# Performance work log

Measured on AMD Instinct MI355X. Metric: run time of the kernel, lower is better.

Reference implementation:

```python
import jax, jax.numpy as jnp
import numpy as np

SHAPE = (4096, 4096)
TAU = 1.0
EPS = 1e-8


def setup_inputs() -> dict:
    key = jax.random.key(0)
    k1, k2, k3 = jax.random.split(key, 3)
    mask_logits = 0.1 * jax.random.normal(k1, SHAPE, dtype=jnp.float32)
    u1 = jax.random.uniform(k2, SHAPE, dtype=jnp.float32)
    u2 = jax.random.uniform(k3, SHAPE + (2,), dtype=jnp.float32)
    return {"mask_logits": mask_logits, "u1": u1, "u2": u2,
            "k": 1677721, "training": 1}


def _gumbel(u):
    # -log(-log(U + eps) + eps), matching the torch code's noise
    return -jnp.log(-jnp.log(u + EPS) + EPS)


def reference(mask_logits, u1, u2, k, training):
    shape = mask_logits.shape
    if training:
        # gumbel-perturbed logits
        logits_with_noise = (mask_logits + _gumbel(u1)) / TAU
        flat = logits_with_noise.reshape(-1)                 # [N]
        _, top_idx = jax.lax.top_k(flat, k)                  # [k]
        # scatter: binary candidate mask (constant values -> non-diff, as in torch)
        mask = jnp.zeros_like(flat).at[top_idx].set(1.0)     # [N]
        # F.gumbel_softmax(stack([0, mask], -1), tau, hard=True)[..., 1]
        logits2 = jnp.stack([jnp.zeros_like(mask), mask], axis=-1)   # [N, 2]
        g2 = _gumbel(u2.reshape(-1, 2))                      # [N, 2]
        y = jax.nn.softmax((logits2 + g2) / TAU, axis=-1)    # soft sample
        hard = jax.nn.one_hot(jnp.argmax(y, axis=-1), 2, dtype=y.dtype)
        out = (hard + y - jax.lax.stop_gradient(y))[..., 1]  # straight-through
        return out.reshape(shape)
    else:
        flat = mask_logits.reshape(-1)
        _, top_idx = jax.lax.top_k(flat, k)
        mask = jnp.zeros_like(flat).at[top_idx].set(1.0)
        return mask.reshape(shape)
```

## Files before the change

kernel.cpp:

```cpp
#include <hip/hip_runtime.h>
#include <hip/hip_bf16.h>
#include <math.h>
#include <cstdint>

#define FEPS 1e-8f
#define NBLK 2048
#define NTHR 256
#define CAND_CAP 4096

#define ZMIN 8.0f
#define ZSCALE 128.0f
#define ZBINW 0.0078125f


__device__ __forceinline__ uint32_t f2k(float f) {
    uint32_t b = __float_as_uint(f);
    return (b & 0x80000000u) ? ~b : (b | 0x80000000u);
}

__device__ __forceinline__ float gum_fast(float u) {
    float t = u + FEPS;
    float a = logf(t);
    float w = -a + FEPS;
    float d = logf(w);
    return -d;
}

__device__ __forceinline__ float logCR(float x) {
    return (float)log((double)x);
}
__device__ __forceinline__ float gum_cr(float u) {
    float t = u + FEPS;
    float a = logCR(t);
    float w = -a + FEPS;
    float d = logCR(w);
    return -d;
}

__device__ __forceinline__ float decide_cr(float maskv, float ua, float ub) {
    float G0 = gum_cr(ua);
    float G1 = gum_cr(ub);
    float V1 = maskv + G1;
    float diff = V1 - G0;
    return (diff > 0x1p-25f) ? 1.0f : 0.0f;
}
__device__ __forceinline__ float decide_tr(float maskv, float ua, float ub) {
    float g0 = gum_fast(ua);
    float g1 = gum_fast(ub);
    float v1 = maskv + g1;
    float diff = v1 - g0;
    if (fabsf(diff) > 1e-4f) return (diff > 0.0f) ? 1.0f : 0.0f;
    return decide_cr(maskv, ua, ub);
}

__device__ __forceinline__ int zbin(float z) {
    float t = (z + ZMIN) * ZSCALE;
    int b = (int)t;
    if (b < 0) b = 0;
    if (b > 4095) b = 4095;
    return b;
}

__global__ void __launch_bounds__(NTHR) k_keys(
        const float* __restrict__ lg, const float* __restrict__ u1,
        const int* __restrict__ trainp, uint32_t* __restrict__ keys,
        uint32_t* __restrict__ hist1, int N) {
    __shared__ uint32_t h[4096];
    for (int b = threadIdx.x; b < 4096; b += blockDim.x) h[b] = 0u;
    __syncthreads();
    const int tr = *trainp;
    const int n4 = N >> 2;
    const int tid = blockIdx.x * blockDim.x + threadIdx.x;
    const int stride = gridDim.x * blockDim.x;
    for (int i = tid; i < n4; i += stride) {
        float4 m = ((const float4*)lg)[i];
        float4 u = ((const float4*)u1)[i];
        float z0, z1, z2, z3;
        if (tr) {
            z0 = m.x + gum_fast(u.x);
            z1 = m.y + gum_fast(u.y);
            z2 = m.z + gum_fast(u.z);
            z3 = m.w + gum_fast(u.w);
        } else { z0 = m.x; z1 = m.y; z2 = m.z; z3 = m.w; }
        uint4 kk = make_uint4(f2k(z0), f2k(z1), f2k(z2), f2k(z3));
        ((uint4*)keys)[i] = kk;
        atomicAdd(&h[zbin(z0)], 1u);
        atomicAdd(&h[zbin(z1)], 1u);
        atomicAdd(&h[zbin(z2)], 1u);
        atomicAdd(&h[zbin(z3)], 1u);
    }
    for (int i = (n4 << 2) + tid; i < N; i += stride) {
        float m = lg[i], u = u1[i];
        float z = tr ? (m + gum_fast(u)) : m;
        keys[i] = f2k(z);
        atomicAdd(&h[zbin(z)], 1u);
    }
    __syncthreads();
    for (int b = threadIdx.x; b < 4096; b += blockDim.x) {
        uint32_t v = h[b];
        if (v) atomicAdd(&hist1[b], v);
    }
}

__global__ void __launch_bounds__(1024) k_scan1(
        const uint32_t* __restrict__ hist1, const int* __restrict__ kptr,
        uint32_t* __restrict__ scal) {
    __shared__ uint32_t vals[4096];
    __shared__ uint32_t cnt[1024];
    const int t = threadIdx.x;
    uint32_t loc = 0;
    for (int j = 0; j < 4; j++) {
        uint32_t v = hist1[4095 - (t * 4 + j)];
        vals[t * 4 + j] = v;
        loc += v;
    }
    cnt[t] = loc;
    __syncthreads();
    for (int off = 1; off < 1024; off <<= 1) {
        uint32_t add = (t >= off) ? cnt[t - off] : 0u;
        __syncthreads();
        cnt[t] += add;
        __syncthreads();
    }
    const uint32_t K = (uint32_t)(*kptr);
    uint32_t excl = (t > 0) ? cnt[t - 1] : 0u;
    uint32_t incl = cnt[t];
    if (excl < K && K <= incl) {
        uint32_t c = excl;
        for (int j = 0; j < 4; j++) {
            uint32_t v = vals[t * 4 + j];
            if (K <= c + v) {
                int b1 = 4095 - (t * 4 + j);
                float edge = (float)b1 * ZBINW - ZMIN;
                uint32_t kb = f2k(edge) - 2048u;
                scal[0] = kb;
                break;
            }
            c += v;
        }
    }
}

__global__ void __launch_bounds__(NTHR) k_hist2(
        const uint32_t* __restrict__ keys, const uint32_t* __restrict__ scal,
        uint32_t* __restrict__ hist2, uint32_t* __restrict__ gtOut, int N) {
    __shared__ uint32_t red[NTHR];
    const uint32_t kb = scal[0];
    const uint32_t hiB = kb + (1u << 20);
    const int n4 = N >> 2;
    const int tid = blockIdx.x * blockDim.x + threadIdx.x;
    const int stride = gridDim.x * blockDim.x;
    uint32_t gt = 0;
    for (int i = tid; i < n4; i += stride) {
        uint4 kk = ((const uint4*)keys)[i];
        uint32_t ks[4] = {kk.x, kk.y, kk.z, kk.w};
        #pragma unroll
        for (int j = 0; j < 4; j++) {
            uint32_t kx = ks[j];
            if (kx >= hiB) gt++;
            else if (kx >= kb) atomicAdd(&hist2[kx - kb], 1u);
        }
    }
    for (int i = (n4 << 2) + tid; i < N; i += stride) {
        uint32_t kx = keys[i];
        if (kx >= hiB) gt++;
        else if (kx >= kb) atomicAdd(&hist2[kx - kb], 1u);
    }
    red[threadIdx.x] = gt;
    __syncthreads();
    for (int off = NTHR / 2; off; off >>= 1) {
        if (threadIdx.x < off) red[threadIdx.x] += red[threadIdx.x + off];
        __syncthreads();
    }
    if (threadIdx.x == 0 && red[0]) atomicAdd(gtOut, red[0]);
}

__global__ void __launch_bounds__(NTHR) k_part(
        const uint32_t* __restrict__ hist2, uint32_t* __restrict__ part) {
    __shared__ uint32_t red[NTHR];
    uint32_t sum = 0;
    const int base = blockIdx.x << 10;
    for (int j = threadIdx.x; j < 1024; j += NTHR) sum += hist2[base + j];
    red[threadIdx.x] = sum;
    __syncthreads();
    for (int off = NTHR / 2; off; off >>= 1) {
        if (threadIdx.x < off) red[threadIdx.x] += red[threadIdx.x + off];
        __syncthreads();
    }
    if (threadIdx.x == 0) part[blockIdx.x] = red[0];
}

__global__ void __launch_bounds__(1024) k_scan2(
        const uint32_t* __restrict__ hist2, const uint32_t* __restrict__ part,
        const int* __restrict__ kptr, uint32_t* __restrict__ scal) {
    __shared__ uint32_t cs[1024];
    __shared__ uint32_t bs[1024];
    __shared__ uint32_t red[1024];
    __shared__ int shI[4];
    const int t = threadIdx.x;
    const uint32_t kb = scal[0];
    const uint32_t GT = scal[1];
    const uint32_t kk1 = (uint32_t)(*kptr) - GT;

    cs[t] = part[1023 - t];
    __syncthreads();
    for (int off = 1; off < 1024; off <<= 1) {
        uint32_t add = (t >= off) ? cs[t - off] : 0u;
        __syncthreads();
        cs[t] += add;
        __syncthreads();
    }
    {
        uint32_t excl = t ? cs[t - 1] : 0u;
        if (excl < kk1 && kk1 <= cs[t]) shI[0] = t;
    }
    __syncthreads();
    const int rp = shI[0];
    const int jc = 1023 - rp;
    const uint32_t gt_chunks = rp ? cs[rp - 1] : 0u;
    const uint32_t kk_in = kk1 - gt_chunks;

    bs[t] = hist2[(jc << 10) + (1023 - t)];
    __syncthreads();
    for (int off = 1; off < 1024; off <<= 1) {
        uint32_t add = (t >= off) ? bs[t - off] : 0u;
        __syncthreads();
        bs[t] += add;
        __syncthreads();
    }
    {
        uint32_t excl = t ? bs[t - 1] : 0u;
        if (excl < kk_in && kk_in <= bs[t]) shI[1] = t;
    }
    __syncthreads();
    const int rq = shI[1];
    const int b2 = (jc << 10) + (1023 - rq);

    int W = 64;
    int lo = 0, hi = 0;
    uint32_t caw = 0;
    while (true) {
        lo = b2 - W; if (lo < 0) lo = 0;
        hi = b2 + W; if (hi > 0xFFFFF) hi = 0xFFFFF;
        uint32_t v = 0;
        for (int b = lo + t; b <= hi; b += 1024) v += hist2[b];
        red[t] = v;
        __syncthreads();
        for (int off = 512; off; off >>= 1) {
            if (t < off) red[t] += red[t + off];
            __syncthreads();
        }
        uint32_t nW = red[0];
        __syncthreads();
        if (nW <= 3500u || W == 0) {
            const int ch = hi >> 10;
            const int chend = (ch << 10) + 1023;
            uint32_t v2 = 0;
            for (int b = hi + 1 + t; b <= chend; b += 1024) v2 += hist2[b];
            red[t] = v2;
            __syncthreads();
            for (int off = 512; off; off >>= 1) {
                if (t < off) red[t] += red[t + off];
                __syncthreads();
            }
            uint32_t inpart = red[0];
            __syncthreads();
            const int rpch = 1023 - ch;
            const uint32_t sufExcl = rpch ? cs[rpch - 1] : 0u;
            caw = GT + sufExcl + inpart;
            break;
        }
        W >>= 1;
    }
    if (t == 0) {
        scal[3] = kb + (uint32_t)lo;
        scal[4] = kb + (uint32_t)hi;
        scal[5] = caw;
    }
}

__global__ void __launch_bounds__(NTHR) k_final(
        uint32_t* __restrict__ keys ,
        const float* __restrict__ u2, const int* __restrict__ trainp,
        const uint32_t* __restrict__ scal,
        uint32_t* __restrict__ candIdx, uint32_t* __restrict__ candCount, int N) {
    const uint32_t klo = scal[3], khi = scal[4];
    const int tr = *trainp;
    const int n4 = N >> 2;
    const int tid = blockIdx.x * blockDim.x + threadIdx.x;
    const int stride = gridDim.x * blockDim.x;
    float* outf = (float*)keys;
    for (int i = tid; i < n4; i += stride) {
        uint4 kk = ((const uint4*)keys)[i];
        uint32_t ks[4] = {kk.x, kk.y, kk.z, kk.w};
        float uu[8];
        if (tr) {
            float4 ua = ((const float4*)u2)[2 * i];
            float4 ub = ((const float4*)u2)[2 * i + 1];
            uu[0] = ua.x; uu[1] = ua.y; uu[2] = ua.z; uu[3] = ua.w;
            uu[4] = ub.x; uu[5] = ub.y; uu[6] = ub.z; uu[7] = ub.w;
        }
        float res[4];
        bool inw[4];
        bool anyw = false;
        #pragma unroll
        for (int j = 0; j < 4; j++) {
            inw[j] = (ks[j] >= klo) && (ks[j] <= khi);
            anyw |= inw[j];
        }
        #pragma unroll
        for (int j = 0; j < 4; j++) {
            float mv = (ks[j] > khi) ? 1.0f : 0.0f;
            res[j] = (tr && !inw[j]) ? decide_tr(mv, uu[2 * j], uu[2 * j + 1]) : mv;
        }
        if (!anyw) {
            ((float4*)outf)[i] = make_float4(res[0], res[1], res[2], res[3]);
        } else {
            #pragma unroll
            for (int j = 0; j < 4; j++) {
                if (inw[j]) {
                    uint32_t p = atomicAdd(candCount, 1u);
                    if (p < CAND_CAP) candIdx[p] = (uint32_t)(4 * i + j);
                } else {
                    outf[4 * i + j] = res[j];
                }
            }
        }
    }
    for (int i = (n4 << 2) + tid; i < N; i += stride) {
        uint32_t kx = keys[i];
        if (kx >= klo && kx <= khi) {
            uint32_t p = atomicAdd(candCount, 1u);
            if (p < CAND_CAP) candIdx[p] = (uint32_t)i;
            continue;
        }
        float mv = (kx > khi) ? 1.0f : 0.0f;
        outf[i] = tr ? decide_tr(mv, u2[2 * i], u2[2 * i + 1]) : mv;
    }
}

__global__ void __launch_bounds__(NTHR) k_refine(
        const float* __restrict__ lg, const float* __restrict__ u1,
        const float* __restrict__ u2, const int* __restrict__ kptr,
        const int* __restrict__ trainp, const uint32_t* __restrict__ scal,
        const uint32_t* __restrict__ candIdx, const uint32_t* __restrict__ candCount,
        float* __restrict__ out) {
    __shared__ float zs[CAND_CAP];
    __shared__ int is[CAND_CAP];
    const int tr = *trainp;
    int n = (int)(*candCount);
    if (n > CAND_CAP) n = CAND_CAP;
    int npow2 = 64;
    while (npow2 < n) npow2 <<= 1;

    for (int e = threadIdx.x; e < npow2; e += NTHR) {
        if (e < n) {
            int i = (int)candIdx[e];
            float m = lg[i];
            zs[e] = tr ? (m + gum_cr(u1[i])) : m;
            is[e] = i;
        } else {
            zs[e] = -INFINITY;
            is[e] = 0x40000000 + e;
        }
    }
    __syncthreads();

    for (int size = 2; size <= npow2; size <<= 1) {
        for (int str = size >> 1; str > 0; str >>= 1) {
            for (int e = threadIdx.x; e < npow2; e += NTHR) {
                int p = e ^ str;
                if (p > e) {
                    float za = zs[e], zb = zs[p];
                    int ia = is[e], ib = is[p];
                    bool aBefore = (za > zb) || (za == zb && ia < ib);
                    bool descBlock = ((e & size) == 0);
                    if (descBlock ? !aBefore : aBefore) {
                        zs[e] = zb; zs[p] = za;
                        is[e] = ib; is[p] = ia;
                    }
                }
            }
            __syncthreads();
        }
    }

    const int K = *kptr;
    const int caw = (int)scal[5];
    const int R = K - caw;
    for (int e = threadIdx.x; e < n; e += NTHR) {
        int i = is[e];
        float mv = (e < R) ? 1.0f : 0.0f;
        float o;
        if (tr) {
            o = decide_cr(mv, u2[2 * i], u2[2 * i + 1]);
        } else {
            o = mv;
        }
        out[i] = o;
    }
}

extern "C" void kernel_launch(void* const* d_in, const int* in_sizes, int n_in,
                              void* d_out, int out_size, void* d_ws, size_t ws_size,
                              hipStream_t stream) {
    const float* lg = (const float*)d_in[0];
    const float* u1 = (const float*)d_in[1];
    const float* u2 = (const float*)d_in[2];
    const int* kptr = (const int*)d_in[3];
    const int* trainp = (const int*)d_in[4];
    float* out = (float*)d_out;
    const int N = in_sizes[0];

    uint32_t* keys = (uint32_t*)d_out;

    uint32_t* hist1 = (uint32_t*)d_ws;
    uint32_t* hist2 = hist1 + 4096;
    uint32_t* part = hist2 + (1u << 20);
    uint32_t* scal = part + 1024;
    uint32_t* candCount = scal + 16;
    uint32_t* candIdx = candCount + 1;

    size_t zero_bytes = (size_t)(4096 + (1u << 20) + 1024 + 16 + 1) * sizeof(uint32_t);
    hipMemsetAsync(d_ws, 0, zero_bytes, stream);

    k_keys<<<dim3(NBLK), dim3(NTHR), 0, stream>>>(lg, u1, trainp, keys, hist1, N);
    k_scan1<<<dim3(1), dim3(1024), 0, stream>>>(hist1, kptr, scal);
    k_hist2<<<dim3(NBLK), dim3(NTHR), 0, stream>>>(keys, scal, hist2, &scal[1], N);
    k_part<<<dim3(1024), dim3(NTHR), 0, stream>>>(hist2, part);
    k_scan2<<<dim3(1), dim3(1024), 0, stream>>>(hist2, part, kptr, scal);
    k_final<<<dim3(NBLK), dim3(NTHR), 0, stream>>>(keys, u2, trainp, scal, candIdx, candCount, N);
    k_refine<<<dim3(1), dim3(NTHR), 0, stream>>>(lg, u1, u2, kptr, trainp, scal, candIdx, candCount, out);
}
```

Measured before the change: 181.1 us.

## Unroll streaming kernels, retune grids, and simplify the Gumbel decision to one log per input

Replaces the per-element hard-sample decision with an algebraically equivalent comparison. It exponentiates through the outer log so each input needs only one logf, using the constant exp(-1) when the mask is set, and falls back to the exact double-precision path near ties. The streaming loops in the key, second-histogram and final kernels are unrolled to process two or four vectors per iteration for more memory-level parallelism. Grid sizes are retuned per kernel. The relative tie threshold changes which elements take the slow exact path, which could affect correctness only if the fallback band is too narrow.

```diff
diff --git a/kernel.cpp b/kernel.cpp
--- a/kernel.cpp
+++ b/kernel.cpp
@@ -4,9 +4,13 @@
 #include <cstdint>
 
 #define FEPS 1e-8f
-#define NBLK 2048
 #define NTHR 256
 #define CAND_CAP 4096
+
+#define GRID_KEYS 2048
+#define GRID_H2   4096
+#define GRID_FIN  8192
+#define GRID_PART 1024
 
 #define ZMIN 8.0f
 #define ZSCALE 128.0f
@@ -44,13 +48,15 @@
     float diff = V1 - G0;
     return (diff > 0x1p-25f) ? 1.0f : 0.0f;
 }
-__device__ __forceinline__ float decide_tr(float maskv, float ua, float ub) {
-    float g0 = gum_fast(ua);
-    float g1 = gum_fast(ub);
-    float v1 = maskv + g1;
-    float diff = v1 - g0;
-    if (fabsf(diff) > 1e-4f) return (diff > 0.0f) ? 1.0f : 0.0f;
-    return decide_cr(maskv, ua, ub);
+
+__device__ __forceinline__ float decide_fast(float mv, float ua, float ub) {
+    float w0 = -logf(ua + FEPS) + FEPS;
+    float w1 = -logf(ub + FEPS) + FEPS;
+    float T = (mv != 0.0f) ? 0.36787944f : 1.0f;
+    float rhs = T * w1;
+    float q = w0 - rhs;
+    if (fabsf(q) > 1e-4f * rhs) return (q > 0.0f) ? 1.0f : 0.0f;
+    return decide_cr(mv, ua, ub);
 }
 
 __device__ __forceinline__ int zbin(float z) {
@@ -66,37 +72,60 @@
         const int* __restrict__ trainp, uint32_t* __restrict__ keys,
         uint32_t* __restrict__ hist1, int N) {
     __shared__ uint32_t h[4096];
-    for (int b = threadIdx.x; b < 4096; b += blockDim.x) h[b] = 0u;
+    for (int b = threadIdx.x; b < 4096; b += NTHR) h[b] = 0u;
     __syncthreads();
     const int tr = *trainp;
     const int n4 = N >> 2;
-    const int tid = blockIdx.x * blockDim.x + threadIdx.x;
-    const int stride = gridDim.x * blockDim.x;
-    for (int i = tid; i < n4; i += stride) {
-        float4 m = ((const float4*)lg)[i];
-        float4 u = ((const float4*)u1)[i];
+    const int nth = gridDim.x * NTHR;
+    const float4* lg4 = (const float4*)lg;
+    const float4* u14 = (const float4*)u1;
+    uint4* k4 = (uint4*)keys;
+
+    int p0 = blockIdx.x * NTHR + threadIdx.x;
+    while (p0 + nth < n4) {
+        const int p1 = p0 + nth;
+        float4 m0 = lg4[p0];
+        float4 m1 = lg4[p1];
+        float4 a0 = u14[p0];
+        float4 a1 = u14[p1];
+        float z0, z1, z2, z3, z4, z5, z6, z7;
+        if (tr) {
+            z0 = m0.x + gum_fast(a0.x); z1 = m0.y + gum_fast(a0.y);
+            z2 = m0.z + gum_fast(a0.z); z3 = m0.w + gum_fast(a0.w);
+            z4 = m1.x + gum_fast(a1.x); z5 = m1.y + gum_fast(a1.y);
+            z6 = m1.z + gum_fast(a1.z); z7 = m1.w + gum_fast(a1.w);
+        } else {
+            z0 = m0.x; z1 = m0.y; z2 = m0.z; z3 = m0.w;
+            z4 = m1.x; z5 = m1.y; z6 = m1.z; z7 = m1.w;
+        }
+        k4[p0] = make_uint4(f2k(z0), f2k(z1), f2k(z2), f2k(z3));
+        k4[p1] = make_uint4(f2k(z4), f2k(z5), f2k(z6), f2k(z7));
+        atomicAdd(&h[zbin(z0)], 1u); atomicAdd(&h[zbin(z1)], 1u);
+        atomicAdd(&h[zbin(z2)], 1u); atomicAdd(&h[zbin(z3)], 1u);
+        atomicAdd(&h[zbin(z4)], 1u); atomicAdd(&h[zbin(z5)], 1u);
+        atomicAdd(&h[zbin(z6)], 1u); atomicAdd(&h[zbin(z7)], 1u);
+        p0 += 2 * nth;
+    }
+    if (p0 < n4) {
+        float4 m0 = lg4[p0];
+        float4 a0 = u14[p0];
         float z0, z1, z2, z3;
         if (tr) {
-            z0 = m.x + gum_fast(u.x);
-            z1 = m.y + gum_fast(u.y);
-            z2 = m.z + gum_fast(u.z);
-            z3 = m.w + gum_fast(u.w);
-        } else { z0 = m.x; z1 = m.y; z2 = m.z; z3 = m.w; }
-        uint4 kk = make_uint4(f2k(z0), f2k(z1), f2k(z2), f2k(z3));
-        ((uint4*)keys)[i] = kk;
-        atomicAdd(&h[zbin(z0)], 1u);
-        atomicAdd(&h[zbin(z1)], 1u);
-        atomicAdd(&h[zbin(z2)], 1u);
-        atomicAdd(&h[zbin(z3)], 1u);
-    }
-    for (int i = (n4 << 2) + tid; i < N; i += stride) {
+            z0 = m0.x + gum_fast(a0.x); z1 = m0.y + gum_fast(a0.y);
+            z2 = m0.z + gum_fast(a0.z); z3 = m0.w + gum_fast(a0.w);
+        } else { z0 = m0.x; z1 = m0.y; z2 = m0.z; z3 = m0.w; }
+        k4[p0] = make_uint4(f2k(z0), f2k(z1), f2k(z2), f2k(z3));
+        atomicAdd(&h[zbin(z0)], 1u); atomicAdd(&h[zbin(z1)], 1u);
+        atomicAdd(&h[zbin(z2)], 1u); atomicAdd(&h[zbin(z3)], 1u);
+    }
+    for (int i = (n4 << 2) + blockIdx.x * NTHR + threadIdx.x; i < N; i += nth) {
         float m = lg[i], u = u1[i];
         float z = tr ? (m + gum_fast(u)) : m;
         keys[i] = f2k(z);
         atomicAdd(&h[zbin(z)], 1u);
     }
     __syncthreads();
-    for (int b = threadIdx.x; b < 4096; b += blockDim.x) {
+    for (int b = threadIdx.x; b < 4096; b += NTHR) {
         uint32_t v = h[b];
         if (v) atomicAdd(&hist1[b], v);
     }
@@ -148,11 +177,28 @@
     const uint32_t kb = scal[0];
     const uint32_t hiB = kb + (1u << 20);
     const int n4 = N >> 2;
-    const int tid = blockIdx.x * blockDim.x + threadIdx.x;
-    const int stride = gridDim.x * blockDim.x;
+    const int nth = gridDim.x * NTHR;
+    const uint4* k4 = (const uint4*)keys;
     uint32_t gt = 0;
-    for (int i = tid; i < n4; i += stride) {
-        uint4 kk = ((const uint4*)keys)[i];
+
+    int p0 = blockIdx.x * NTHR + threadIdx.x;
+    while (p0 + 3 * nth < n4) {
+        uint4 kk0 = k4[p0];
+        uint4 kk1 = k4[p0 + nth];
+        uint4 kk2 = k4[p0 + 2 * nth];
+        uint4 kk3 = k4[p0 + 3 * nth];
+        uint32_t ks[16] = {kk0.x, kk0.y, kk0.z, kk0.w, kk1.x, kk1.y, kk1.z, kk1.w,
+                           kk2.x, kk2.y, kk2.z, kk2.w, kk3.x, kk3.y, kk3.z, kk3.w};
+        #pragma unroll
+        for (int j = 0; j < 16; j++) {
+            uint32_t kx = ks[j];
+            if (kx >= hiB) gt++;
+            else if (kx >= kb) atomicAdd(&hist2[kx - kb], 1u);
+        }
+        p0 += 4 * nth;
+    }
+    while (p0 < n4) {
+        uint4 kk = k4[p0];
         uint32_t ks[4] = {kk.x, kk.y, kk.z, kk.w};
         #pragma unroll
         for (int j = 0; j < 4; j++) {
@@ -160,8 +206,9 @@
             if (kx >= hiB) gt++;
             else if (kx >= kb) atomicAdd(&hist2[kx - kb], 1u);
         }
-    }
-    for (int i = (n4 << 2) + tid; i < N; i += stride) {
+        p0 += nth;
+    }
+    for (int i = (n4 << 2) + blockIdx.x * NTHR + threadIdx.x; i < N; i += nth) {
         uint32_t kx = keys[i];
         if (kx >= hiB) gt++;
         else if (kx >= kb) atomicAdd(&hist2[kx - kb], 1u);
@@ -287,47 +334,82 @@
     const uint32_t klo = scal[3], khi = scal[4];
     const int tr = *trainp;
     const int n4 = N >> 2;
-    const int tid = blockIdx.x * blockDim.x + threadIdx.x;
-    const int stride = gridDim.x * blockDim.x;
+    const int nth = gridDim.x * NTHR;
+    const uint4* kr4 = (const uint4*)keys;
+    const float4* u24 = (const float4*)u2;
     float* outf = (float*)keys;
-    for (int i = tid; i < n4; i += stride) {
-        uint4 kk = ((const uint4*)keys)[i];
-        uint32_t ks[4] = {kk.x, kk.y, kk.z, kk.w};
-        float uu[8];
+
+    int p0 = blockIdx.x * NTHR + threadIdx.x;
+    while (p0 + nth < n4) {
+        const int p1 = p0 + nth;
+        uint4 kk0 = kr4[p0];
+        uint4 kk1 = kr4[p1];
+        float4 ua0, ub0, ua1, ub1;
         if (tr) {
-            float4 ua = ((const float4*)u2)[2 * i];
-            float4 ub = ((const float4*)u2)[2 * i + 1];
-            uu[0] = ua.x; uu[1] = ua.y; uu[2] = ua.z; uu[3] = ua.w;
-            uu[4] = ub.x; uu[5] = ub.y; uu[6] = ub.z; uu[7] = ub.w;
-        }
-        float res[4];
-        bool inw[4];
+            ua0 = u24[2 * p0]; ub0 = u24[2 * p0 + 1];
+            ua1 = u24[2 * p1]; ub1 = u24[2 * p1 + 1];
+        }
+        uint32_t ks[8] = {kk0.x, kk0.y, kk0.z, kk0.w, kk1.x, kk1.y, kk1.z, kk1.w};
+        float uu[16];
+        if (tr) {
+            uu[0] = ua0.x; uu[1] = ua0.y; uu[2] = ua0.z; uu[3] = ua0.w;
+            uu[4] = ub0.x; uu[5] = ub0.y; uu[6] = ub0.z; uu[7] = ub0.w;
+            uu[8] = ua1.x; uu[9] = ua1.y; uu[10] = ua1.z; uu[11] = ua1.w;
+            uu[12] = ub1.x; uu[13] = ub1.y; uu[14] = ub1.z; uu[15] = ub1.w;
+        }
+        float res[8];
+        bool inw[8];
         bool anyw = false;
         #pragma unroll
-        for (int j = 0; j < 4; j++) {
+        for (int j = 0; j < 8; j++) {
             inw[j] = (ks[j] >= klo) && (ks[j] <= khi);
             anyw |= inw[j];
         }
         #pragma unroll
-        for (int j = 0; j < 4; j++) {
+        for (int j = 0; j < 8; j++) {
+            const int half = j >> 2, e = j & 3;
             float mv = (ks[j] > khi) ? 1.0f : 0.0f;
-            res[j] = (tr && !inw[j]) ? decide_tr(mv, uu[2 * j], uu[2 * j + 1]) : mv;
+            float ua = uu[half * 8 + 2 * e];
+            float ub = uu[half * 8 + 2 * e + 1];
+            res[j] = (tr && !inw[j]) ? decide_fast(mv, ua, ub) : mv;
         }
         if (!anyw) {
-            ((float4*)outf)[i] = make_float4(res[0], res[1], res[2], res[3]);
+            ((float4*)outf)[p0] = make_float4(res[0], res[1], res[2], res[3]);
+            ((float4*)outf)[p1] = make_float4(res[4], res[5], res[6], res[7]);
         } else {
             #pragma unroll
-            for (int j = 0; j < 4; j++) {
+            for (int j = 0; j < 8; j++) {
+                const int idx = ((j < 4) ? p0 : p1) * 4 + (j & 3);
                 if (inw[j]) {
                     uint32_t p = atomicAdd(candCount, 1u);
-                    if (p < CAND_CAP) candIdx[p] = (uint32_t)(4 * i + j);
+                    if (p < CAND_CAP) candIdx[p] = (uint32_t)idx;
                 } else {
-                    outf[4 * i + j] = res[j];
+                    outf[idx] = res[j];
                 }
             }
         }
-    }
-    for (int i = (n4 << 2) + tid; i < N; i += stride) {
+        p0 += 2 * nth;
+    }
+    if (p0 < n4) {
+        uint4 kk = kr4[p0];
+        float4 ua, ub;
+        if (tr) { ua = u24[2 * p0]; ub = u24[2 * p0 + 1]; }
+        uint32_t ks[4] = {kk.x, kk.y, kk.z, kk.w};
+        float pa[4] = {ua.x, ua.z, ub.x, ub.z};
+        float pb[4] = {ua.y, ua.w, ub.y, ub.w};
+        #pragma unroll
+        for (int j = 0; j < 4; j++) {
+            uint32_t kx = ks[j];
+            if (kx >= klo && kx <= khi) {
+                uint32_t p = atomicAdd(candCount, 1u);
+                if (p < CAND_CAP) candIdx[p] = (uint32_t)(4 * p0 + j);
+            } else {
+                float mv = (kx > khi) ? 1.0f : 0.0f;
+                outf[4 * p0 + j] = tr ? decide_fast(mv, pa[j], pb[j]) : mv;
+            }
+        }
+    }
+    for (int i = (n4 << 2) + blockIdx.x * NTHR + threadIdx.x; i < N; i += nth) {
         uint32_t kx = keys[i];
         if (kx >= klo && kx <= khi) {
             uint32_t p = atomicAdd(candCount, 1u);
@@ -335,7 +417,7 @@
             continue;
         }
         float mv = (kx > khi) ? 1.0f : 0.0f;
-        outf[i] = tr ? decide_tr(mv, u2[2 * i], u2[2 * i + 1]) : mv;
+        outf[i] = tr ? decide_fast(mv, u2[2 * i], u2[2 * i + 1]) : mv;
     }
 }
 
@@ -391,13 +473,7 @@
     for (int e = threadIdx.x; e < n; e += NTHR) {
         int i = is[e];
         float mv = (e < R) ? 1.0f : 0.0f;
-        float o;
-        if (tr) {
-            o = decide_cr(mv, u2[2 * i], u2[2 * i + 1]);
-        } else {
-            o = mv;
-        }
-        out[i] = o;
+        out[i] = tr ? decide_cr(mv, u2[2 * i], u2[2 * i + 1]) : mv;
     }
 }
 
@@ -424,11 +500,11 @@
     size_t zero_bytes = (size_t)(4096 + (1u << 20) + 1024 + 16 + 1) * sizeof(uint32_t);
     hipMemsetAsync(d_ws, 0, zero_bytes, stream);
 
-    k_keys<<<dim3(NBLK), dim3(NTHR), 0, stream>>>(lg, u1, trainp, keys, hist1, N);
+    k_keys<<<dim3(GRID_KEYS), dim3(NTHR), 0, stream>>>(lg, u1, trainp, keys, hist1, N);
     k_scan1<<<dim3(1), dim3(1024), 0, stream>>>(hist1, kptr, scal);
-    k_hist2<<<dim3(NBLK), dim3(NTHR), 0, stream>>>(keys, scal, hist2, &scal[1], N);
-    k_part<<<dim3(1024), dim3(NTHR), 0, stream>>>(hist2, part);
+    k_hist2<<<dim3(GRID_H2), dim3(NTHR), 0, stream>>>(keys, scal, hist2, &scal[1], N);
+    k_part<<<dim3(GRID_PART), dim3(NTHR), 0, stream>>>(hist2, part);
     k_scan2<<<dim3(1), dim3(1024), 0, stream>>>(hist2, part, kptr, scal);
-    k_final<<<dim3(NBLK), dim3(NTHR), 0, stream>>>(keys, u2, trainp, scal, candIdx, candCount, N);
+    k_final<<<dim3(GRID_FIN), dim3(NTHR), 0, stream>>>(keys, u2, trainp, scal, candIdx, candCount, N);
     k_refine<<<dim3(1), dim3(NTHR), 0, stream>>>(lg, u1, u2, kptr, trainp, scal, candIdx, candCount, out);
 }
```

New measurement: 189.4 us. +4.6%, slower.
